# Optimization experiments

Hardware: AMD Instinct MI355X
Metric: run time of the kernel (lower is better)

Reference implementation:

```python
import jax, jax.numpy as jnp
import numpy as np

N_NODES = 100000   # vertices
N_EDGES = 20000    # hyperedges
NNZ = 1600000      # incidence entries (avg vertex degree 16)
D_IN = 128
D_OUT = 128


def setup_inputs() -> dict:
    key = jax.random.key(0)
    k1, k2, k3, k4, k5 = jax.random.split(key, 5)
    X = jax.random.normal(k1, (N_NODES, D_IN), dtype=jnp.float32)
    v_idx = jax.random.randint(k2, (NNZ,), 0, N_NODES)
    e_idx = jax.random.randint(k3, (NNZ,), 0, N_EDGES)
    theta_w = jax.random.normal(k4, (D_IN, D_OUT), dtype=jnp.float32) / np.sqrt(D_IN)
    theta_b = jax.random.normal(k5, (D_OUT,), dtype=jnp.float32) * 0.01
    return {"X": X, "theta_w": theta_w, "theta_b": theta_b,
            "v_idx": v_idx, "e_idx": e_idx}


def reference(X, theta_w, theta_b, v_idx, e_idx):
    # degrees (edge weights w_e = 1)
    ones = jnp.ones(v_idx.shape[0], dtype=X.dtype)
    d_v = jax.ops.segment_sum(ones, v_idx, num_segments=N_NODES)   # [N]
    d_e = jax.ops.segment_sum(ones, e_idx, num_segments=N_EDGES)   # [M]
    inv_sqrt_dv = jnp.where(d_v > 0, d_v ** -0.5, 0.0)
    inv_de = jnp.where(d_e > 0, 1.0 / d_e, 0.0)

    # theta: dense GEMM
    Xt = X @ theta_w + theta_b                                     # [N, D_OUT]

    # smoothing_with_HGNN: D_v^{-1/2} H W D_e^{-1} H^T D_v^{-1/2} Xt
    Xs = Xt * inv_sqrt_dv[:, None]                                 # [N, D_OUT]
    Ye = jax.ops.segment_sum(Xs[v_idx], e_idx, num_segments=N_EDGES)  # H^T Xs -> [M, D_OUT]
    Ye = Ye * inv_de[:, None]
    Xv = jax.ops.segment_sum(Ye[e_idx], v_idx, num_segments=N_NODES)  # H Ye -> [N, D_OUT]
    return jax.nn.relu(Xv * inv_sqrt_dv[:, None])
```

## Files before the change

kernel.cpp:

```cpp
#include <hip/hip_runtime.h>

#define N_NODES 100000
#define N_EDGES 20000
#define NNZ     1600000
#define D       128
#define DW      64

#define NB      256
#define CAP_E   8192
#define CAP_V   8192
#define SPAN_E  ((N_EDGES + NB - 1) / NB)
#define SPAN_V  ((N_NODES + NB - 1) / NB)
#define P1_CHUNK 2048
#define P1_ITER  (P1_CHUNK / 256)
#define P1_BLOCKS ((NNZ + P1_CHUNK - 1) / P1_CHUNK)

__device__ __forceinline__ unsigned int pack_bf2(float lo, float hi) {
  unsigned int ul = __float_as_uint(lo), uh = __float_as_uint(hi);
  ul = (ul + 0x7FFFu + ((ul >> 16) & 1u)) >> 16;
  uh = (uh + 0x7FFFu + ((uh >> 16) & 1u)) & 0xFFFF0000u;
  return ul | uh;
}

__global__ void k_init(int* __restrict__ ce, int* __restrict__ cv) {
  int t = threadIdx.x;
  ce[t] = t * CAP_E;
  cv[t] = t * CAP_V;
}

__global__ __launch_bounds__(256) void k_bin(const int* __restrict__ v_idx, const int* __restrict__ e_idx,
                                             int* __restrict__ ce, int* __restrict__ cv,
                                             unsigned int* __restrict__ Te, unsigned int* __restrict__ Tv) {
  __shared__ int he[NB], hv[NB], be[NB], bv[NB], le[NB], lv[NB];
  int t = threadIdx.x;
  he[t] = 0; hv[t] = 0; le[t] = 0; lv[t] = 0;
  __syncthreads();
  int base = blockIdx.x * P1_CHUNK;
  int v[P1_ITER], e[P1_ITER];
#pragma unroll
  for (int j = 0; j < P1_ITER; ++j) {
    int idx = base + j * 256 + t;
    if (idx < NNZ) {
      v[j] = v_idx[idx]; e[j] = e_idx[idx];
      atomicAdd(&he[e[j] / SPAN_E], 1);
      atomicAdd(&hv[v[j] / SPAN_V], 1);
    } else v[j] = -1;
  }
  __syncthreads();
  be[t] = he[t] ? atomicAdd(&ce[t], he[t]) : 0;
  bv[t] = hv[t] ? atomicAdd(&cv[t], hv[t]) : 0;
  __syncthreads();
#pragma unroll
  for (int j = 0; j < P1_ITER; ++j) {
    if (v[j] < 0) continue;
    int eb = e[j] / SPAN_E, vb = v[j] / SPAN_V;
    int se = be[eb] + atomicAdd(&le[eb], 1);
    int sv = bv[vb] + atomicAdd(&lv[vb], 1);
    if (se < (eb + 1) * CAP_E) Te[se] = ((unsigned)e[j] << 17) | (unsigned)v[j];
    if (sv < (vb + 1) * CAP_V) Tv[sv] = ((unsigned)v[j] << 15) | (unsigned)e[j];
  }
}

__global__ __launch_bounds__(256) void k_sort_v(const int* __restrict__ cv, unsigned int* __restrict__ Tv,
                                                int* __restrict__ cnt_v, float* __restrict__ risv,
                                                int* __restrict__ starts_v,
                                                const float* __restrict__ X, unsigned int* __restrict__ Xs) {
  __shared__ unsigned int raw[CAP_V];
  __shared__ int hist[SPAN_V], lcur[SPAN_V], loff[SPAN_V + 1];
  __shared__ float rv[SPAN_V];
  int b = blockIdx.x, t = threadIdx.x;
  int v0 = b * SPAN_V;
  int span = N_NODES - v0; if (span > SPAN_V) span = SPAN_V;
  if (span <= 0) return;
  int n = cv[b] - b * CAP_V; if (n > CAP_V) n = CAP_V; if (n < 0) n = 0;
  for (int i = t; i < n; i += 256) raw[i] = Tv[b * CAP_V + i];
  for (int i = t; i < span; i += 256) { hist[i] = 0; lcur[i] = 0; }
  __syncthreads();
  for (int i = t; i < n; i += 256) atomicAdd(&hist[(int)(raw[i] >> 15) - v0], 1);
  __syncthreads();
  if (t == 0) { int run = 0; for (int i = 0; i < span; ++i) { loff[i] = run; run += hist[i]; } loff[span] = run; }
  __syncthreads();
  for (int i = t; i < n; i += 256) {
    unsigned int p = raw[i];
    int l = (int)(p >> 15) - v0;
    int slot = loff[l] + atomicAdd(&lcur[l], 1);
    Tv[b * CAP_V + slot] = p & 0x7FFFu;
  }
  for (int i = t; i < span; i += 256) {
    int d = hist[i];
    float r = d > 0 ? rsqrtf((float)d) : 0.0f;
    cnt_v[v0 + i] = d;
    risv[v0 + i] = r;
    rv[i] = r;
    starts_v[v0 + i] = b * CAP_V + loff[i];
  }
  __syncthreads();
  int total = span * DW;
  for (int idx = t; idx < total; idx += 256) {
    int vl = idx >> 6;
    float r = rv[vl];
    size_t gp = (size_t)(v0 + vl) * DW + (idx & 63);
    float2 x = *(const float2*)(X + gp * 2);
    Xs[gp] = pack_bf2(r * x.x, r * x.y);
  }
}

__global__ __launch_bounds__(256) void k_sort_e(const int* __restrict__ ce, unsigned int* __restrict__ Te,
                                                const float* __restrict__ risv,
                                                int* __restrict__ cnt_e, float* __restrict__ invde,
                                                int* __restrict__ starts_e, float* __restrict__ qv) {
  __shared__ unsigned int raw[CAP_E];
  __shared__ int hist[SPAN_E], lcur[SPAN_E], loff[SPAN_E + 1];
  __shared__ float qacc[SPAN_E];
  int b = blockIdx.x, t = threadIdx.x;
  int e0 = b * SPAN_E;
  int span = N_EDGES - e0; if (span > SPAN_E) span = SPAN_E;
  if (span <= 0) return;
  int n = ce[b] - b * CAP_E; if (n > CAP_E) n = CAP_E; if (n < 0) n = 0;
  for (int i = t; i < n; i += 256) raw[i] = Te[b * CAP_E + i];
  for (int i = t; i < span; i += 256) { hist[i] = 0; lcur[i] = 0; qacc[i] = 0.f; }
  __syncthreads();
  for (int i = t; i < n; i += 256) atomicAdd(&hist[(int)(raw[i] >> 17) - e0], 1);
  __syncthreads();
  if (t == 0) { int run = 0; for (int i = 0; i < span; ++i) { loff[i] = run; run += hist[i]; } loff[span] = run; }
  __syncthreads();
  for (int i = t; i < n; i += 256) {
    unsigned int p = raw[i];
    int l = (int)(p >> 17) - e0;
    int vtx = (int)(p & 0x1FFFFu);
    int slot = loff[l] + atomicAdd(&lcur[l], 1);
    Te[b * CAP_E + slot] = (unsigned)vtx;
    atomicAdd(&qacc[l], risv[vtx]);
  }
  __syncthreads();
  for (int i = t; i < span; i += 256) {
    int d = hist[i];
    cnt_e[e0 + i] = d;
    invde[e0 + i] = d > 0 ? 1.0f / (float)d : 0.0f;
    starts_e[e0 + i] = b * CAP_E + loff[i];
    qv[e0 + i] = qacc[i];
  }
}

__global__ void k_edge_gather(const unsigned int* __restrict__ Xs,
                              const int* __restrict__ starts_e, const int* __restrict__ cnt_e,
                              const unsigned int* __restrict__ members,
                              unsigned int* __restrict__ Qeb) {
  int wid = (blockIdx.x * 256 + threadIdx.x) >> 6;
  int lane = threadIdx.x & 63;
  if (wid >= N_EDGES) return;
  int beg = __builtin_amdgcn_readfirstlane(starts_e[wid]);
  int end = beg + __builtin_amdgcn_readfirstlane(cnt_e[wid]);
  float ax = 0.f, ay = 0.f;
  int i = beg;
  for (; i + 16 <= end; i += 16) {
    int vv[16]; unsigned int xx[16];
#pragma unroll
    for (int j = 0; j < 16; ++j) vv[j] = members[i + j];
#pragma unroll
    for (int j = 0; j < 16; ++j) xx[j] = Xs[(size_t)vv[j] * DW + lane];
#pragma unroll
    for (int j = 0; j < 16; ++j) {
      ax += __uint_as_float(xx[j] << 16);
      ay += __uint_as_float(xx[j] & 0xFFFF0000u);
    }
  }
  if (i + 8 <= end) {
    int vv[8]; unsigned int xx[8];
#pragma unroll
    for (int j = 0; j < 8; ++j) vv[j] = members[i + j];
#pragma unroll
    for (int j = 0; j < 8; ++j) xx[j] = Xs[(size_t)vv[j] * DW + lane];
#pragma unroll
    for (int j = 0; j < 8; ++j) {
      ax += __uint_as_float(xx[j] << 16);
      ay += __uint_as_float(xx[j] & 0xFFFF0000u);
    }
    i += 8;
  }
  for (; i < end; ++i) {
    unsigned int x = Xs[(size_t)members[i] * DW + lane];
    ax += __uint_as_float(x << 16);
    ay += __uint_as_float(x & 0xFFFF0000u);
  }
  Qeb[(size_t)wid * DW + lane] = pack_bf2(ax, ay);
}

__global__ __launch_bounds__(256) void k_gemm(const unsigned int* __restrict__ Qeb, const float* __restrict__ qv,
                                              const float* __restrict__ W, const float* __restrict__ bias,
                                              const float* __restrict__ invde, unsigned int* __restrict__ Yeb) {
  __shared__ float Wl[D * D];
  __shared__ float bl[D];
  __shared__ float Ql[16][130];
  int tid = threadIdx.x;
  const float4* W4 = (const float4*)W;
  float4* Wl4 = (float4*)Wl;
#pragma unroll
  for (int j = 0; j < 16; ++j) Wl4[tid + 256 * j] = W4[tid + 256 * j];
  if (tid < 32) ((float4*)bl)[tid] = ((const float4*)bias)[tid];
  int row0 = blockIdx.x * 16;
  const unsigned int* Q8 = Qeb + (size_t)row0 * DW;
#pragma unroll
  for (int j = 0; j < 4; ++j) {
    int idx = tid + 256 * j;
    int r = idx >> 6, c = idx & 63;
    unsigned int u = Q8[idx];
    Ql[r][2 * c]     = __uint_as_float(u << 16);
    Ql[r][2 * c + 1] = __uint_as_float(u & 0xFFFF0000u);
  }
  __syncthreads();
  int ty = tid >> 4, tx = tid & 15;
  float acc[8];
#pragma unroll
  for (int j = 0; j < 8; ++j) acc[j] = 0.f;
#pragma unroll 4
  for (int k = 0; k < D; ++k) {
    float xv = Ql[ty][k];
    const float* wr = Wl + k * D + tx * 8;
#pragma unroll
    for (int j = 0; j < 8; ++j) acc[j] += xv * wr[j];
  }
  int row = row0 + ty;
  float s = invde[row]; float q = qv[row];
  unsigned int* orow = Yeb + (size_t)row * DW + tx * 4;
#pragma unroll
  for (int j = 0; j < 4; ++j) {
    float lo = s * (acc[2 * j]     + q * bl[tx * 8 + 2 * j]);
    float hi = s * (acc[2 * j + 1] + q * bl[tx * 8 + 2 * j + 1]);
    orow[j] = pack_bf2(lo, hi);
  }
}

__global__ void k_vertex_gather(const unsigned int* __restrict__ Yeb, const float* __restrict__ risv,
                                const int* __restrict__ starts_v, const int* __restrict__ cnt_v,
                                const unsigned int* __restrict__ members,
                                float* __restrict__ out) {
  int wid = (blockIdx.x * 256 + threadIdx.x) >> 6;
  int lane = threadIdx.x & 63;
  if (wid >= N_NODES) return;
  int beg = __builtin_amdgcn_readfirstlane(starts_v[wid]);
  int end = beg + __builtin_amdgcn_readfirstlane(cnt_v[wid]);
  float ax = 0.f, ay = 0.f;
  int i = beg;
  for (; i + 16 <= end; i += 16) {
    int ee[16]; unsigned int yy[16];
#pragma unroll
    for (int j = 0; j < 16; ++j) ee[j] = members[i + j];
#pragma unroll
    for (int j = 0; j < 16; ++j) yy[j] = Yeb[(size_t)ee[j] * DW + lane];
#pragma unroll
    for (int j = 0; j < 16; ++j) {
      ax += __uint_as_float(yy[j] << 16);
      ay += __uint_as_float(yy[j] & 0xFFFF0000u);
    }
  }
  if (i + 8 <= end) {
    int ee[8]; unsigned int yy[8];
#pragma unroll
    for (int j = 0; j < 8; ++j) ee[j] = members[i + j];
#pragma unroll
    for (int j = 0; j < 8; ++j) yy[j] = Yeb[(size_t)ee[j] * DW + lane];
#pragma unroll
    for (int j = 0; j < 8; ++j) {
      ax += __uint_as_float(yy[j] << 16);
      ay += __uint_as_float(yy[j] & 0xFFFF0000u);
    }
    i += 8;
  }
  for (; i < end; ++i) {
    unsigned int y = Yeb[(size_t)members[i] * DW + lane];
    ax += __uint_as_float(y << 16);
    ay += __uint_as_float(y & 0xFFFF0000u);
  }
  float s = risv[wid];
  float2 o; o.x = fmaxf(ax * s, 0.f); o.y = fmaxf(ay * s, 0.f);
  *(float2*)(out + (size_t)wid * D + lane * 2) = o;
}

extern "C" void kernel_launch(void* const* d_in, const int* in_sizes, int n_in,
                              void* d_out, int out_size, void* d_ws, size_t ws_size,
                              hipStream_t stream) {
  const float* X    = (const float*)d_in[0];
  const float* W    = (const float*)d_in[1];
  const float* bias = (const float*)d_in[2];
  const int* v_idx  = (const int*)d_in[3];
  const int* e_idx  = (const int*)d_in[4];
  float* out = (float*)d_out;

  char* p = (char*)d_ws;
  auto alloc = [&](size_t bytes) { char* r = p; p += (bytes + 255) & ~(size_t)255; return r; };
  unsigned int* Te  = (unsigned int*)alloc((size_t)NB * CAP_E * 4);
  unsigned int* Tv  = (unsigned int*)alloc((size_t)NB * CAP_V * 4);
  unsigned int* Xs  = (unsigned int*)alloc((size_t)N_NODES * DW * 4);
  unsigned int* Qeb = (unsigned int*)alloc((size_t)N_EDGES * DW * 4);
  unsigned int* Yeb = (unsigned int*)alloc((size_t)N_EDGES * DW * 4);
  float* qv    = (float*)alloc((size_t)N_EDGES * 4);
  float* risv  = (float*)alloc((size_t)N_NODES * 4);
  float* invde = (float*)alloc((size_t)N_EDGES * 4);
  int* cnt_e    = (int*)alloc((size_t)N_EDGES * 4);
  int* cnt_v    = (int*)alloc((size_t)N_NODES * 4);
  int* starts_e = (int*)alloc((size_t)N_EDGES * 4);
  int* starts_v = (int*)alloc((size_t)N_NODES * 4);
  int* ce       = (int*)alloc(NB * 4);
  int* cv       = (int*)alloc(NB * 4);

  k_init<<<1, NB, 0, stream>>>(ce, cv);
  k_bin<<<P1_BLOCKS, 256, 0, stream>>>(v_idx, e_idx, ce, cv, Te, Tv);
  k_sort_v<<<NB, 256, 0, stream>>>(cv, Tv, cnt_v, risv, starts_v, X, Xs);
  k_sort_e<<<NB, 256, 0, stream>>>(ce, Te, risv, cnt_e, invde, starts_e, qv);

  k_edge_gather<<<N_EDGES / 4, 256, 0, stream>>>(Xs, starts_e, cnt_e, Te, Qeb);
  k_gemm<<<N_EDGES / 16, 256, 0, stream>>>(Qeb, qv, W, bias, invde, Yeb);
  k_vertex_gather<<<N_NODES / 4, 256, 0, stream>>>(Yeb, risv, starts_v, cnt_v, Tv, out);
}
```

Measured before the change: 317.8 us.

## Use bf16 MFMA for edge GEMM, merge sort kernels, move qv into gather

Replaces the FP32 shared-memory GEMM with a per-wave bf16 MFMA 16x16x32 kernel, using a W pre-packed in k_prep into a transposed bf16 layout. The vertex and edge sort kernels merge into one launch of 2*NB blocks. The per-edge sum of inverse-sqrt degrees moves from the edge sort into the edge gather. The k_bin chunk size grows from 2048 to 8192 entries per block. Together these cut launches and the cost of the GEMM and sort stages, at the price of bf16 rounding of W in the GEMM and fewer binning blocks.

```diff
diff --git a/kernel.cpp b/kernel.cpp
--- a/kernel.cpp
+++ b/kernel.cpp
@@ -11,9 +11,12 @@
 #define CAP_V   8192
 #define SPAN_E  ((N_EDGES + NB - 1) / NB)
 #define SPAN_V  ((N_NODES + NB - 1) / NB)
-#define P1_CHUNK 2048
+#define P1_CHUNK 8192
 #define P1_ITER  (P1_CHUNK / 256)
 #define P1_BLOCKS ((NNZ + P1_CHUNK - 1) / P1_CHUNK)
+
+typedef __attribute__((ext_vector_type(8))) short bf16x8;
+typedef __attribute__((ext_vector_type(4))) float f32x4;
 
 __device__ __forceinline__ unsigned int pack_bf2(float lo, float hi) {
   unsigned int ul = __float_as_uint(lo), uh = __float_as_uint(hi);
@@ -22,10 +25,17 @@
   return ul | uh;
 }
 
-__global__ void k_init(int* __restrict__ ce, int* __restrict__ cv) {
+__global__ __launch_bounds__(256) void k_prep(const float* __restrict__ W, unsigned int* __restrict__ Wtp,
+                                              int* __restrict__ ce, int* __restrict__ cv) {
   int t = threadIdx.x;
-  ce[t] = t * CAP_E;
-  cv[t] = t * CAP_V;
+  if (blockIdx.x == 0) { ce[t] = t * CAP_E; cv[t] = t * CAP_V; }
+  int idx = blockIdx.x * 256 + t;
+  if (idx < D * DW) {
+    int c = idx & 127, kp = idx >> 7;
+    float lo = W[(size_t)(2 * kp) * D + c];
+    float hi = W[(size_t)(2 * kp + 1) * D + c];
+    Wtp[c * DW + kp] = pack_bf2(lo, hi);
+  }
 }
 
 __global__ __launch_bounds__(256) void k_bin(const int* __restrict__ v_idx, const int* __restrict__ e_idx,
@@ -61,97 +71,91 @@
   }
 }
 
-__global__ __launch_bounds__(256) void k_sort_v(const int* __restrict__ cv, unsigned int* __restrict__ Tv,
-                                                int* __restrict__ cnt_v, float* __restrict__ risv,
-                                                int* __restrict__ starts_v,
-                                                const float* __restrict__ X, unsigned int* __restrict__ Xs) {
+__global__ __launch_bounds__(256) void k_sort(const int* __restrict__ ce, const int* __restrict__ cv,
+                                              unsigned int* __restrict__ Te, unsigned int* __restrict__ Tv,
+                                              int* __restrict__ cnt_e, float* __restrict__ invde,
+                                              int* __restrict__ starts_e,
+                                              int* __restrict__ cnt_v, float* __restrict__ risv,
+                                              int* __restrict__ starts_v,
+                                              const float* __restrict__ X, unsigned int* __restrict__ Xs) {
   __shared__ unsigned int raw[CAP_V];
   __shared__ int hist[SPAN_V], lcur[SPAN_V], loff[SPAN_V + 1];
   __shared__ float rv[SPAN_V];
-  int b = blockIdx.x, t = threadIdx.x;
-  int v0 = b * SPAN_V;
-  int span = N_NODES - v0; if (span > SPAN_V) span = SPAN_V;
-  if (span <= 0) return;
-  int n = cv[b] - b * CAP_V; if (n > CAP_V) n = CAP_V; if (n < 0) n = 0;
-  for (int i = t; i < n; i += 256) raw[i] = Tv[b * CAP_V + i];
-  for (int i = t; i < span; i += 256) { hist[i] = 0; lcur[i] = 0; }
-  __syncthreads();
-  for (int i = t; i < n; i += 256) atomicAdd(&hist[(int)(raw[i] >> 15) - v0], 1);
-  __syncthreads();
-  if (t == 0) { int run = 0; for (int i = 0; i < span; ++i) { loff[i] = run; run += hist[i]; } loff[span] = run; }
-  __syncthreads();
-  for (int i = t; i < n; i += 256) {
-    unsigned int p = raw[i];
-    int l = (int)(p >> 15) - v0;
-    int slot = loff[l] + atomicAdd(&lcur[l], 1);
-    Tv[b * CAP_V + slot] = p & 0x7FFFu;
-  }
-  for (int i = t; i < span; i += 256) {
-    int d = hist[i];
-    float r = d > 0 ? rsqrtf((float)d) : 0.0f;
-    cnt_v[v0 + i] = d;
-    risv[v0 + i] = r;
-    rv[i] = r;
-    starts_v[v0 + i] = b * CAP_V + loff[i];
-  }
-  __syncthreads();
-  int total = span * DW;
-  for (int idx = t; idx < total; idx += 256) {
-    int vl = idx >> 6;
-    float r = rv[vl];
-    size_t gp = (size_t)(v0 + vl) * DW + (idx & 63);
-    float2 x = *(const float2*)(X + gp * 2);
-    Xs[gp] = pack_bf2(r * x.x, r * x.y);
-  }
-}
-
-__global__ __launch_bounds__(256) void k_sort_e(const int* __restrict__ ce, unsigned int* __restrict__ Te,
-                                                const float* __restrict__ risv,
-                                                int* __restrict__ cnt_e, float* __restrict__ invde,
-                                                int* __restrict__ starts_e, float* __restrict__ qv) {
-  __shared__ unsigned int raw[CAP_E];
-  __shared__ int hist[SPAN_E], lcur[SPAN_E], loff[SPAN_E + 1];
-  __shared__ float qacc[SPAN_E];
-  int b = blockIdx.x, t = threadIdx.x;
-  int e0 = b * SPAN_E;
-  int span = N_EDGES - e0; if (span > SPAN_E) span = SPAN_E;
-  if (span <= 0) return;
-  int n = ce[b] - b * CAP_E; if (n > CAP_E) n = CAP_E; if (n < 0) n = 0;
-  for (int i = t; i < n; i += 256) raw[i] = Te[b * CAP_E + i];
-  for (int i = t; i < span; i += 256) { hist[i] = 0; lcur[i] = 0; qacc[i] = 0.f; }
-  __syncthreads();
-  for (int i = t; i < n; i += 256) atomicAdd(&hist[(int)(raw[i] >> 17) - e0], 1);
-  __syncthreads();
-  if (t == 0) { int run = 0; for (int i = 0; i < span; ++i) { loff[i] = run; run += hist[i]; } loff[span] = run; }
-  __syncthreads();
-  for (int i = t; i < n; i += 256) {
-    unsigned int p = raw[i];
-    int l = (int)(p >> 17) - e0;
-    int vtx = (int)(p & 0x1FFFFu);
-    int slot = loff[l] + atomicAdd(&lcur[l], 1);
-    Te[b * CAP_E + slot] = (unsigned)vtx;
-    atomicAdd(&qacc[l], risv[vtx]);
-  }
-  __syncthreads();
-  for (int i = t; i < span; i += 256) {
-    int d = hist[i];
-    cnt_e[e0 + i] = d;
-    invde[e0 + i] = d > 0 ? 1.0f / (float)d : 0.0f;
-    starts_e[e0 + i] = b * CAP_E + loff[i];
-    qv[e0 + i] = qacc[i];
-  }
-}
-
-__global__ void k_edge_gather(const unsigned int* __restrict__ Xs,
+  int t = threadIdx.x;
+  if (blockIdx.x < NB) {
+    int b = blockIdx.x;
+    int v0 = b * SPAN_V;
+    int span = N_NODES - v0; if (span > SPAN_V) span = SPAN_V;
+    if (span <= 0) return;
+    int n = cv[b] - b * CAP_V; if (n > CAP_V) n = CAP_V; if (n < 0) n = 0;
+    for (int i = t; i < n; i += 256) raw[i] = Tv[b * CAP_V + i];
+    for (int i = t; i < span; i += 256) { hist[i] = 0; lcur[i] = 0; }
+    __syncthreads();
+    for (int i = t; i < n; i += 256) atomicAdd(&hist[(int)(raw[i] >> 15) - v0], 1);
+    __syncthreads();
+    if (t == 0) { int run = 0; for (int i = 0; i < span; ++i) { loff[i] = run; run += hist[i]; } loff[span] = run; }
+    __syncthreads();
+    for (int i = t; i < n; i += 256) {
+      unsigned int p = raw[i];
+      int l = (int)(p >> 15) - v0;
+      int slot = loff[l] + atomicAdd(&lcur[l], 1);
+      Tv[b * CAP_V + slot] = p & 0x7FFFu;
+    }
+    for (int i = t; i < span; i += 256) {
+      int d = hist[i];
+      float r = d > 0 ? rsqrtf((float)d) : 0.0f;
+      cnt_v[v0 + i] = d;
+      risv[v0 + i] = r;
+      rv[i] = r;
+      starts_v[v0 + i] = b * CAP_V + loff[i];
+    }
+    __syncthreads();
+    int total = span * DW;
+    for (int idx = t; idx < total; idx += 256) {
+      int vl = idx >> 6;
+      float r = rv[vl];
+      size_t gp = (size_t)(v0 + vl) * DW + (idx & 63);
+      float2 x = *(const float2*)(X + gp * 2);
+      Xs[gp] = pack_bf2(r * x.x, r * x.y);
+    }
+  } else {
+    int b = blockIdx.x - NB;
+    int e0 = b * SPAN_E;
+    int span = N_EDGES - e0; if (span > SPAN_E) span = SPAN_E;
+    if (span <= 0) return;
+    int n = ce[b] - b * CAP_E; if (n > CAP_E) n = CAP_E; if (n < 0) n = 0;
+    for (int i = t; i < n; i += 256) raw[i] = Te[b * CAP_E + i];
+    for (int i = t; i < span; i += 256) { hist[i] = 0; lcur[i] = 0; }
+    __syncthreads();
+    for (int i = t; i < n; i += 256) atomicAdd(&hist[(int)(raw[i] >> 17) - e0], 1);
+    __syncthreads();
+    if (t == 0) { int run = 0; for (int i = 0; i < span; ++i) { loff[i] = run; run += hist[i]; } loff[span] = run; }
+    __syncthreads();
+    for (int i = t; i < n; i += 256) {
+      unsigned int p = raw[i];
+      int l = (int)(p >> 17) - e0;
+      int slot = loff[l] + atomicAdd(&lcur[l], 1);
+      Te[b * CAP_E + slot] = p & 0x1FFFFu;
+    }
+    for (int i = t; i < span; i += 256) {
+      int d = hist[i];
+      cnt_e[e0 + i] = d;
+      invde[e0 + i] = d > 0 ? 1.0f / (float)d : 0.0f;
+      starts_e[e0 + i] = b * CAP_E + loff[i];
+    }
+  }
+}
+
+__global__ void k_edge_gather(const unsigned int* __restrict__ Xs, const float* __restrict__ risv,
                               const int* __restrict__ starts_e, const int* __restrict__ cnt_e,
                               const unsigned int* __restrict__ members,
-                              unsigned int* __restrict__ Qeb) {
+                              unsigned int* __restrict__ Qeb, float* __restrict__ qv) {
   int wid = (blockIdx.x * 256 + threadIdx.x) >> 6;
   int lane = threadIdx.x & 63;
   if (wid >= N_EDGES) return;
   int beg = __builtin_amdgcn_readfirstlane(starts_e[wid]);
   int end = beg + __builtin_amdgcn_readfirstlane(cnt_e[wid]);
-  float ax = 0.f, ay = 0.f;
+  float ax = 0.f, ay = 0.f, q = 0.f;
   int i = beg;
   for (; i + 16 <= end; i += 16) {
     int vv[16]; unsigned int xx[16];
@@ -160,6 +164,8 @@
 #pragma unroll
     for (int j = 0; j < 16; ++j) xx[j] = Xs[(size_t)vv[j] * DW + lane];
 #pragma unroll
+    for (int j = 0; j < 16; ++j) q += risv[vv[j]];
+#pragma unroll
     for (int j = 0; j < 16; ++j) {
       ax += __uint_as_float(xx[j] << 16);
       ay += __uint_as_float(xx[j] & 0xFFFF0000u);
@@ -172,6 +178,8 @@
 #pragma unroll
     for (int j = 0; j < 8; ++j) xx[j] = Xs[(size_t)vv[j] * DW + lane];
 #pragma unroll
+    for (int j = 0; j < 8; ++j) q += risv[vv[j]];
+#pragma unroll
     for (int j = 0; j < 8; ++j) {
       ax += __uint_as_float(xx[j] << 16);
       ay += __uint_as_float(xx[j] & 0xFFFF0000u);
@@ -179,55 +187,49 @@
     i += 8;
   }
   for (; i < end; ++i) {
-    unsigned int x = Xs[(size_t)members[i] * DW + lane];
+    int v = members[i];
+    unsigned int x = Xs[(size_t)v * DW + lane];
     ax += __uint_as_float(x << 16);
     ay += __uint_as_float(x & 0xFFFF0000u);
+    q += risv[v];
   }
   Qeb[(size_t)wid * DW + lane] = pack_bf2(ax, ay);
+  if (lane == 0) qv[wid] = q;
 }
 
 __global__ __launch_bounds__(256) void k_gemm(const unsigned int* __restrict__ Qeb, const float* __restrict__ qv,
-                                              const float* __restrict__ W, const float* __restrict__ bias,
-                                              const float* __restrict__ invde, unsigned int* __restrict__ Yeb) {
-  __shared__ float Wl[D * D];
-  __shared__ float bl[D];
-  __shared__ float Ql[16][130];
-  int tid = threadIdx.x;
-  const float4* W4 = (const float4*)W;
-  float4* Wl4 = (float4*)Wl;
-#pragma unroll
-  for (int j = 0; j < 16; ++j) Wl4[tid + 256 * j] = W4[tid + 256 * j];
-  if (tid < 32) ((float4*)bl)[tid] = ((const float4*)bias)[tid];
-  int row0 = blockIdx.x * 16;
-  const unsigned int* Q8 = Qeb + (size_t)row0 * DW;
-#pragma unroll
-  for (int j = 0; j < 4; ++j) {
-    int idx = tid + 256 * j;
-    int r = idx >> 6, c = idx & 63;
-    unsigned int u = Q8[idx];
-    Ql[r][2 * c]     = __uint_as_float(u << 16);
-    Ql[r][2 * c + 1] = __uint_as_float(u & 0xFFFF0000u);
-  }
-  __syncthreads();
-  int ty = tid >> 4, tx = tid & 15;
-  float acc[8];
-#pragma unroll
-  for (int j = 0; j < 8; ++j) acc[j] = 0.f;
-#pragma unroll 4
-  for (int k = 0; k < D; ++k) {
-    float xv = Ql[ty][k];
-    const float* wr = Wl + k * D + tx * 8;
-#pragma unroll
-    for (int j = 0; j < 8; ++j) acc[j] += xv * wr[j];
-  }
-  int row = row0 + ty;
-  float s = invde[row]; float q = qv[row];
-  unsigned int* orow = Yeb + (size_t)row * DW + tx * 4;
-#pragma unroll
-  for (int j = 0; j < 4; ++j) {
-    float lo = s * (acc[2 * j]     + q * bl[tx * 8 + 2 * j]);
-    float hi = s * (acc[2 * j + 1] + q * bl[tx * 8 + 2 * j + 1]);
-    orow[j] = pack_bf2(lo, hi);
+                                              const unsigned int* __restrict__ Wtp, const float* __restrict__ bias,
+                                              const float* __restrict__ invde, unsigned short* __restrict__ Yeb) {
+  int wid = (blockIdx.x * 256 + threadIdx.x) >> 6;
+  int lane = threadIdx.x & 63;
+  if (wid >= N_EDGES / 16) return;
+  int e0 = wid * 16;
+  int lrow = lane & 15, lhalf = lane >> 4;
+  const unsigned int* arow = Qeb + (size_t)(e0 + lrow) * DW + lhalf * 4;
+  f32x4 acc[8];
+#pragma unroll
+  for (int nt = 0; nt < 8; ++nt) acc[nt] = (f32x4){0.f, 0.f, 0.f, 0.f};
+#pragma unroll
+  for (int kt = 0; kt < 4; ++kt) {
+    bf16x8 a = *(const bf16x8*)(arow + kt * 16);
+#pragma unroll
+    for (int nt = 0; nt < 8; ++nt) {
+      bf16x8 b = *(const bf16x8*)(Wtp + (size_t)(nt * 16 + lrow) * DW + kt * 16 + lhalf * 4);
+      acc[nt] = __builtin_amdgcn_mfma_f32_16x16x32_bf16(a, b, acc[nt], 0, 0, 0);
+    }
+  }
+#pragma unroll
+  for (int r = 0; r < 4; ++r) {
+    int row = e0 + lhalf * 4 + r;
+    float s = invde[row], q = qv[row];
+#pragma unroll
+    for (int nt = 0; nt < 8; ++nt) {
+      int c = nt * 16 + lrow;
+      float val = s * (acc[nt][r] + q * bias[c]);
+      unsigned int u = __float_as_uint(val);
+      u = (u + 0x7FFFu + ((u >> 16) & 1u)) >> 16;
+      Yeb[(size_t)row * D + c] = (unsigned short)u;
+    }
   }
 }
 
@@ -294,6 +296,7 @@
   unsigned int* Xs  = (unsigned int*)alloc((size_t)N_NODES * DW * 4);
   unsigned int* Qeb = (unsigned int*)alloc((size_t)N_EDGES * DW * 4);
   unsigned int* Yeb = (unsigned int*)alloc((size_t)N_EDGES * DW * 4);
+  unsigned int* Wtp = (unsigned int*)alloc((size_t)D * DW * 4);
   float* qv    = (float*)alloc((size_t)N_EDGES * 4);
   float* risv  = (float*)alloc((size_t)N_NODES * 4);
   float* invde = (float*)alloc((size_t)N_EDGES * 4);
@@ -304,12 +307,11 @@
   int* ce       = (int*)alloc(NB * 4);
   int* cv       = (int*)alloc(NB * 4);
 
-  k_init<<<1, NB, 0, stream>>>(ce, cv);
+  k_prep<<<(D * DW + 255) / 256, 256, 0, stream>>>(W, Wtp, ce, cv);
   k_bin<<<P1_BLOCKS, 256, 0, stream>>>(v_idx, e_idx, ce, cv, Te, Tv);
-  k_sort_v<<<NB, 256, 0, stream>>>(cv, Tv, cnt_v, risv, starts_v, X, Xs);
-  k_sort_e<<<NB, 256, 0, stream>>>(ce, Te, risv, cnt_e, invde, starts_e, qv);
-
-  k_edge_gather<<<N_EDGES / 4, 256, 0, stream>>>(Xs, starts_e, cnt_e, Te, Qeb);
-  k_gemm<<<N_EDGES / 16, 256, 0, stream>>>(Qeb, qv, W, bias, invde, Yeb);
+  k_sort<<<2 * NB, 256, 0, stream>>>(ce, cv, Te, Tv, cnt_e, invde, starts_e,
+                                     cnt_v, risv, starts_v, X, Xs);
+  k_edge_gather<<<N_EDGES / 4, 256, 0, stream>>>(Xs, risv, starts_e, cnt_e, Te, Qeb, qv);
+  k_gemm<<<(N_EDGES / 16 + 3) / 4, 256, 0, stream>>>(Qeb, qv, Wtp, bias, invde, (unsigned short*)Yeb);
   k_vertex_gather<<<N_NODES / 4, 256, 0, stream>>>(Yeb, risv, starts_v, cnt_v, Tv, out);
 }
```

Measured after the change: 289.5 us. -8.9%, faster.
